# Performance work log

Measured on AMD Instinct MI355X. Metric: run time of the kernel, lower is better.

The kernel has to match this reference:

```python
import jax, jax.numpy as jnp
import numpy as np


def _consts():
    # Hypercube vertices: itertools.product([-1,1], repeat=n) order => MSB-first bits.
    def verts(nbits):
        idx = np.arange(2 ** nbits)
        return (((idx[:, None] >> np.arange(nbits - 1, -1, -1)[None, :]) & 1) * 2.0 - 1.0).astype(np.float32)

    hexagrams = verts(6)   # (64, 6)
    q2_verts = verts(2)    # (4, 2)
    q3_verts = verts(3)    # (8, 3)

    # Q2 vertex -> group one-hot, _Q2_TO_GROUP = [2, 1, 1, 0]
    q2_to_group = np.zeros((4, 3), dtype=np.float32)
    for v, g in enumerate([2, 1, 1, 0]):
        q2_to_group[v, g] = 1.0

    # Group anchors: ABSTRACT = mean(hex[63], hex[62]), DYNAMIC = mean(hex[19], hex[21]),
    # CONCRETE = mean(hex[0], hex[8]); then L2-normalized.
    anch = np.stack([
        hexagrams[[63, 62]].mean(0),
        hexagrams[[19, 21]].mean(0),
        hexagrams[[0, 8]].mean(0),
    ]).astype(np.float32)
    anch = anch / np.clip(np.linalg.norm(anch, axis=-1, keepdims=True), 1e-12, None)

    # Walsh-Hadamard popcount masks, pre-divided by their sums -> (64, 3) matrix.
    bits = np.array([bin(i).count('1') for i in range(64)], dtype=np.float32)
    wa = (bits >= 5).astype(np.float32)
    wd = (bits == 3).astype(np.float32)
    wc = (bits <= 1).astype(np.float32)
    wht_mat = np.stack([wa / wa.sum(), wd / wd.sum(), wc / wc.sum()], axis=1)

    return tuple(jnp.asarray(a) for a in (hexagrams, q2_verts, q3_verts, q2_to_group, anch, wht_mat))


def _q3_to_group_init():
    q3_map = np.zeros((8, 3), dtype=np.float32)
    for i in range(8):
        yc = bin(i).count('1')
        if yc == 0:
            q3_map[i, 2] = 1.0
        elif yc == 1:
            q3_map[i, 1] = 1.0
        elif yc == 2:
            q3_map[i, 0] = 0.6
            q3_map[i, 1] = 0.4
        else:
            q3_map[i, 0] = 1.0
    q3_map = q3_map / np.clip(q3_map.sum(axis=1, keepdims=True), 1e-8, None)
    return q3_map


def setup_inputs() -> dict:
    key = jax.random.key(0)
    k_x, k2, k3, k6 = jax.random.split(key, 4)
    B, T, D = 4, 4096, 2048
    s = 1.0 / float(np.sqrt(D))  # torch Linear default init range
    return {
        'x': jax.random.normal(k_x, (B, T, D), dtype=jnp.float32),
        'ln_w': jnp.ones((D,), dtype=jnp.float32),
        'ln_b': jnp.zeros((D,), dtype=jnp.float32),
        'w_q2': jax.random.uniform(k2, (2, D), minval=-s, maxval=s, dtype=jnp.float32),
        'w_q3': jax.random.uniform(k3, (3, D), minval=-s, maxval=s, dtype=jnp.float32),
        'w_q6': jax.random.uniform(k6, (6, D), minval=-s, maxval=s, dtype=jnp.float32),
        'log_temp': jnp.asarray(np.log(0.5), dtype=jnp.float32),
        'log_scale_mix': jnp.zeros((3,), dtype=jnp.float32),
        'q3_to_group': jnp.asarray(_q3_to_group_init()),
        'log_wht_mix': jnp.asarray(-2.0, dtype=jnp.float32),
    }


def _forward(x, ln_w, ln_b, w_q2, w_q3, w_q6, log_temp, log_scale_mix, q3_to_group, log_wht_mix):
    hexa, q2v, q3v, q2g, anch, wht_mat = _consts()

    # LayerNorm (eps = 1e-5, torch default)
    mu = x.mean(-1, keepdims=True)
    var = ((x - mu) ** 2).mean(-1, keepdims=True)
    h = (x - mu) * jax.lax.rsqrt(var + 1e-5) * ln_w + ln_b

    temp = jnp.clip(jnp.exp(log_temp), 0.1, 5.0)

    # Q2 scale: (B,T,2) -> 4 vertices -> 3 groups
    w2 = jax.nn.softmax(jnp.tanh(h @ w_q2.T) @ q2v.T / temp, axis=-1)
    score_q2 = w2 @ q2g

    # Q3 scale: (B,T,3) -> 8 vertices -> learned soft group map
    w3 = jax.nn.softmax(jnp.tanh(h @ w_q3.T) @ q3v.T / temp, axis=-1)
    score_q3 = w3 @ jax.nn.softmax(q3_to_group, axis=-1)

    # Q6 scale: (B,T,6) -> 64 hexagram vertices
    hex_w = jax.nn.softmax(jnp.tanh(h @ w_q6.T) @ hexa.T / temp, axis=-1)
    score_cos = (hex_w @ hexa) @ anch.T            # cosine-sim vs normalized anchors
    score_wht = hex_w @ wht_mat                    # popcount-mask averages
    alpha = jax.nn.sigmoid(log_wht_mix)
    score_q6 = (1.0 - alpha) * score_cos + alpha * score_wht

    mix = jax.nn.softmax(log_scale_mix)
    group_w = jax.nn.softmax(mix[0] * score_q2 + mix[1] * score_q3 + mix[2] * score_q6, axis=-1)

    mg = group_w.mean(axis=(0, 1))
    mh = hex_w.mean(axis=(0, 1))
    lb_loss = jnp.sum(mg * jnp.log(mg + 1e-8)) + 0.1 * jnp.sum(mh * jnp.log(mh + 1e-8))
    return group_w, hex_w, lb_loss


def reference(x, ln_w, ln_b, w_q2, w_q3, w_q6, log_temp, log_scale_mix, q3_to_group, log_wht_mix):
    return _forward(x, ln_w, ln_b, w_q2, w_q3, w_q6, log_temp, log_scale_mix, q3_to_group, log_wht_mix)
```

## Files before the change

### kernel.cpp

```cpp
#include <hip/hip_runtime.h>
#include <math.h>
#include <string.h>

#define D 2048
#define NTOK 16384
#define NROW 11
#define MROWS_U32 (NROW * D / 2)
#define K1_BLOCKS 2048
#define K1_THREADS 256
#define P1_ROWS 6
#define P2_ROWS 5
#define SW_U32 (P1_ROWS * 1024)

#define WS_A 0
#define WS_B 16
#define WS_IT 32
#define WS_ALPHA 33
#define WS_MIX 34
#define WS_M3 40
#define WS_MERGED 64
#define WS_PART (WS_MERGED + MROWS_U32)

typedef __fp16 h2 __attribute__((ext_vector_type(2)));

__device__ __forceinline__ float wsum(float v){
#pragma unroll
  for (int m = 1; m < 64; m <<= 1) v += __shfl_xor(v, m, 64);
  return v;
}
__device__ __forceinline__ float wmax(float v){
#pragma unroll
  for (int m = 1; m < 64; m <<= 1) v = fmaxf(v, __shfl_xor(v, m, 64));
  return v;
}
__device__ __forceinline__ float rcp_fast(float x){ return __builtin_amdgcn_rcpf(x); }
__device__ __forceinline__ float tanh_fast(float x){
  float e = __expf(2.0f * x);
  return 1.0f - 2.0f * rcp_fast(e + 1.0f);
}
__device__ __forceinline__ float sload(const float* __restrict__ p){
  return __uint_as_float(__builtin_amdgcn_readfirstlane(__float_as_uint(*p)));
}
__device__ __forceinline__ h2 u2h(unsigned int u){ h2 h; memcpy(&h, &u, 4); return h; }
__device__ __forceinline__ unsigned int h2u(h2 h){ unsigned int u; memcpy(&u, &h, 4); return u; }

__device__ __forceinline__ float fdot2(h2 a, h2 b, float c){
#if __has_builtin(__builtin_amdgcn_fdot2)
  return __builtin_amdgcn_fdot2(a, b, c, false);
#else
  return fmaf((float)a[0], (float)b[0], fmaf((float)a[1], (float)b[1], c));
#endif
}

__global__ __launch_bounds__(256) void k0_prep(
    const float* __restrict__ ln_w, const float* __restrict__ ln_b,
    const float* __restrict__ w_q2, const float* __restrict__ w_q3,
    const float* __restrict__ w_q6,
    const float* __restrict__ log_temp, const float* __restrict__ log_scale_mix,
    const float* __restrict__ q3_to_group, const float* __restrict__ log_wht_mix,
    float* __restrict__ ws)
{
  const int tid = threadIdx.x;
  const int k = blockIdx.x;
  unsigned int* wsu = (unsigned int*)ws;
  if (k < NROW){
    const float* row = (k < 2) ? (w_q2 + (size_t)k * D)
                     : (k < 5) ? (w_q3 + (size_t)(k - 2) * D)
                               : (w_q6 + (size_t)(k - 5) * D);
    float pa = 0.f, pb = 0.f;
    for (int i = tid * 2; i < D; i += 512){
      float w0 = row[i], w1 = row[i + 1];
      h2 h = __builtin_amdgcn_cvt_pkrtz(ln_w[i] * w0, ln_w[i + 1] * w1);
      pa += (float)h[0] + (float)h[1];
      pb = fmaf(ln_b[i], w0, pb);
      pb = fmaf(ln_b[i + 1], w1, pb);
      wsu[WS_MERGED + k * 1024 + i / 2] = h2u(h);
    }
    __shared__ float red[8];
    pa = wsum(pa); pb = wsum(pb);
    if ((tid & 63) == 0){ red[tid >> 6] = pa; red[4 + (tid >> 6)] = pb; }
    __syncthreads();
    if (tid == 0){
      ws[WS_A + k] = red[0] + red[1] + red[2] + red[3];
      ws[WS_B + k] = red[4] + red[5] + red[6] + red[7];
    }
  } else if (tid == 0){
    float t = __expf(log_temp[0]);
    t = fminf(fmaxf(t, 0.1f), 5.0f);
    ws[WS_IT] = 1.0f / t;
    ws[WS_ALPHA] = 1.0f / (1.0f + __expf(-log_wht_mix[0]));
    float m0 = log_scale_mix[0], m1 = log_scale_mix[1], m2 = log_scale_mix[2];
    float mm = fmaxf(m0, fmaxf(m1, m2));
    float e0 = __expf(m0 - mm), e1 = __expf(m1 - mm), e2 = __expf(m2 - mm);
    float inv = 1.0f / (e0 + e1 + e2);
    ws[WS_MIX + 0] = e0 * inv; ws[WS_MIX + 1] = e1 * inv; ws[WS_MIX + 2] = e2 * inv;
    for (int r = 0; r < 8; ++r){
      float v0 = q3_to_group[r*3+0], v1 = q3_to_group[r*3+1], v2 = q3_to_group[r*3+2];
      float mx = fmaxf(v0, fmaxf(v1, v2));
      float f0 = __expf(v0 - mx), f1 = __expf(v1 - mx), f2 = __expf(v2 - mx);
      float iv = 1.0f / (f0 + f1 + f2);
      ws[WS_M3 + r*3 + 0] = f0 * iv;
      ws[WS_M3 + r*3 + 1] = f1 * iv;
      ws[WS_M3 + r*3 + 2] = f2 * iv;
    }
  }
}

template<int NR>
__device__ __forceinline__ void dot_phase(const unsigned int* __restrict__ sW,
                                          const h2* __restrict__ xah,
                                          const h2* __restrict__ xbh,
                                          float* __restrict__ t0,
                                          float* __restrict__ t1, int lane){
#pragma unroll
  for (int c = 0; c < 8; ++c){
    const unsigned int* wb = sW + (c << 7) + lane * 2;
    const h2 a0 = xah[2*c], a1 = xah[2*c + 1];
    const h2 b0 = xbh[2*c], b1 = xbh[2*c + 1];
#pragma unroll
    for (int r = 0; r < NR; ++r){
      uint2 wu = *(const uint2*)(wb + (r << 10));
      h2 w0 = u2h(wu.x), w1 = u2h(wu.y);
      t0[r] = fdot2(a0, w0, t0[r]);
      t0[r] = fdot2(a1, w1, t0[r]);
      t1[r] = fdot2(b0, w0, t1[r]);
      t1[r] = fdot2(b1, w1, t1[r]);
    }
  }
}

__global__ __launch_bounds__(256) void k1_main(
    const float* __restrict__ x, const float* __restrict__ ws,
    float* __restrict__ gout, float* __restrict__ hout, float* __restrict__ part)
{
  __shared__ unsigned int sW[SW_U32];
  __shared__ float lred[4][68];
  const int tid  = threadIdx.x;
  const int lane = tid & 63;
  const int wid  = tid >> 6;
  const int blk  = blockIdx.x;
  const int tok0 = blk * 8 + wid * 2;

  const unsigned int* wsu = (const unsigned int*)ws + WS_MERGED;

  const float* xp0 = x + (size_t)tok0 * D + lane * 4;
  const float* xp1 = xp0 + D;
  float4 xa[8], xb[8];
#pragma unroll
  for (int i = 0; i < 8; ++i) xa[i] = *(const float4*)(xp0 + i * 256);
#pragma unroll
  for (int i = 0; i < 8; ++i) xb[i] = *(const float4*)(xp1 + i * 256);

  {
    const uint4* src = (const uint4*)wsu;
    uint4* dst = (uint4*)sW;
#pragma unroll
    for (int i = 0; i < 6; ++i) dst[tid + i * 256] = src[tid + i * 256];
  }

  float sum0 = 0.f, sum1 = 0.f, sq0 = 0.f, sq1 = 0.f;
  h2 xah[16], xbh[16];
#pragma unroll
  for (int i = 0; i < 8; ++i){
    float a0 = xa[i].x, a1 = xa[i].y, a2 = xa[i].z, a3 = xa[i].w;
    sum0 += (a0 + a1) + (a2 + a3);
    sq0 = fmaf(a0,a0, fmaf(a1,a1, fmaf(a2,a2, fmaf(a3,a3, sq0))));
    xah[2*i]   = __builtin_amdgcn_cvt_pkrtz(a0, a1);
    xah[2*i+1] = __builtin_amdgcn_cvt_pkrtz(a2, a3);
    float b0 = xb[i].x, b1 = xb[i].y, b2 = xb[i].z, b3 = xb[i].w;
    sum1 += (b0 + b1) + (b2 + b3);
    sq1 = fmaf(b0,b0, fmaf(b1,b1, fmaf(b2,b2, fmaf(b3,b3, sq1))));
    xbh[2*i]   = __builtin_amdgcn_cvt_pkrtz(b0, b1);
    xbh[2*i+1] = __builtin_amdgcn_cvt_pkrtz(b2, b3);
  }
  __syncthreads();

  float t0a[P1_ROWS], t1a[P1_ROWS];
#pragma unroll
  for (int r = 0; r < P1_ROWS; ++r){ t0a[r] = 0.f; t1a[r] = 0.f; }
  dot_phase<P1_ROWS>(sW, xah, xbh, t0a, t1a, lane);

  sum0 = wsum(sum0); sum1 = wsum(sum1);
  sq0  = wsum(sq0);  sq1  = wsum(sq1);
#pragma unroll
  for (int r = 0; r < P1_ROWS; ++r){ t0a[r] = wsum(t0a[r]); t1a[r] = wsum(t1a[r]); }

  __syncthreads();

  {
    const uint4* src = (const uint4*)(wsu + P1_ROWS * 1024);
    uint4* dst = (uint4*)sW;
#pragma unroll
    for (int i = 0; i < 5; ++i) dst[tid + i * 256] = src[tid + i * 256];
  }
  __syncthreads();

  float t0b[P2_ROWS], t1b[P2_ROWS];
#pragma unroll
  for (int r = 0; r < P2_ROWS; ++r){ t0b[r] = 0.f; t1b[r] = 0.f; }
  dot_phase<P2_ROWS>(sW, xah, xbh, t0b, t1b, lane);
#pragma unroll
  for (int r = 0; r < P2_ROWS; ++r){ t0b[r] = wsum(t0b[r]); t1b[r] = wsum(t1b[r]); }

  float a[NROW], bb[NROW];
#pragma unroll
  for (int k = 0; k < NROW; ++k){ a[k] = sload(ws + WS_A + k); bb[k] = sload(ws + WS_B + k); }
  const float it    = sload(ws + WS_IT);
  const float alpha = sload(ws + WS_ALPHA);
  const float mix0 = sload(ws + WS_MIX), mix1 = sload(ws + WS_MIX + 1), mix2 = sload(ws + WS_MIX + 2);
  float M3r[8][3];
#pragma unroll
  for (int r = 0; r < 8; ++r){
#pragma unroll
    for (int g = 0; g < 3; ++g) M3r[r][g] = sload(ws + WS_M3 + r*3 + g);
  }

  float sgn[6];
#pragma unroll
  for (int j = 0; j < 6; ++j) sgn[j] = ((lane >> (5 - j)) & 1) ? 1.0f : -1.0f;
  const float C5 = 0.44721359549995793f;
  const float A0c[6] = { C5,  C5,  C5,  C5,  C5, 0.f };
  const float A1c[6] = {-0.5f, 0.5f, -0.5f, 0.f, 0.f, 0.5f};
  const float A2c[6] = {-C5, -C5, 0.f, -C5, -C5, -C5};
  float cs0 = 0.f, cs1 = 0.f, cs2 = 0.f;
#pragma unroll
  for (int j = 0; j < 6; ++j){
    cs0 = fmaf(sgn[j], A0c[j], cs0);
    cs1 = fmaf(sgn[j], A1c[j], cs1);
    cs2 = fmaf(sgn[j], A2c[j], cs2);
  }
  const int pc = __popc(lane);
  const float w7c = 1.0f / 7.0f;
  float wh0 = (pc >= 5) ? w7c  : 0.f;
  float wh1 = (pc == 3) ? 0.05f: 0.f;
  float wh2 = (pc <= 1) ? w7c  : 0.f;
  const float m60 = (1.f - alpha)*cs0 + alpha*wh0;
  const float m61 = (1.f - alpha)*cs1 + alpha*wh1;
  const float m62 = (1.f - alpha)*cs2 + alpha*wh2;

  float hsum = 0.f, ga0 = 0.f, ga1 = 0.f, ga2 = 0.f;

#pragma unroll
  for (int j = 0; j < 2; ++j){
    const int tok = tok0 + j;
    const float sumj = j ? sum1 : sum0;
    const float sqj  = j ? sq1  : sq0;
    float mean = sumj * (1.0f / D);
    float var  = fmaf(sqj, 1.0f / D, -mean * mean);
    float rr   = rsqrtf(var + 1e-5f);
    float u[NROW];
#pragma unroll
    for (int k = 0; k < NROW; ++k){
      float tk = (k < P1_ROWS) ? (j ? t1a[k] : t0a[k]) : (j ? t1b[k - P1_ROWS] : t0b[k - P1_ROWS]);
      float d = fmaf(-mean, a[k], tk);
      u[k] = tanh_fast(fmaf(rr, d, bb[k]));
    }

    float p01 = u[0] + u[1], m01 = u[0] - u[1];
    float l0 = -p01*it, l1 = -m01*it, l2 = m01*it, l3 = p01*it;
    float mx2 = fmaxf(fmaxf(l0, l1), fmaxf(l2, l3));
    float e0 = __expf(l0-mx2), e1 = __expf(l1-mx2), e2 = __expf(l2-mx2), e3 = __expf(l3-mx2);
    float i2 = rcp_fast(e0 + e1 + e2 + e3);
    float s2g0 = e3 * i2, s2g1 = (e1 + e2) * i2, s2g2 = e0 * i2;

    float l3v[8]; float mx3 = -1e30f;
#pragma unroll
    for (int v = 0; v < 8; ++v){
      float acc = ((v & 4) ? u[2] : -u[2]) + ((v & 2) ? u[3] : -u[3]) + ((v & 1) ? u[4] : -u[4]);
      l3v[v] = acc * it;
      mx3 = fmaxf(mx3, l3v[v]);
    }
    float w3v[8]; float se3 = 0.f;
#pragma unroll
    for (int v = 0; v < 8; ++v){ w3v[v] = __expf(l3v[v] - mx3); se3 += w3v[v]; }
    float i3 = rcp_fast(se3);
    float s3g0 = 0.f, s3g1 = 0.f, s3g2 = 0.f;
#pragma unroll
    for (int v = 0; v < 8; ++v){
      s3g0 = fmaf(w3v[v], M3r[v][0], s3g0);
      s3g1 = fmaf(w3v[v], M3r[v][1], s3g1);
      s3g2 = fmaf(w3v[v], M3r[v][2], s3g2);
    }
    s3g0 *= i3; s3g1 *= i3; s3g2 *= i3;

    float lg = 0.f;
#pragma unroll
    for (int jj = 0; jj < 6; ++jj) lg = fmaf(sgn[jj], u[5 + jj], lg);
    lg *= it;
    float mx6 = wmax(lg);
    float p   = __expf(lg - mx6);
    float se6 = wsum(p);
    float hw  = p * rcp_fast(se6);
    hout[(size_t)tok * 64 + lane] = hw;
    hsum += hw;
    float s6g0 = wsum(hw * m60);
    float s6g1 = wsum(hw * m61);
    float s6g2 = wsum(hw * m62);

    float g0 = mix0*s2g0 + mix1*s3g0 + mix2*s6g0;
    float g1 = mix0*s2g1 + mix1*s3g1 + mix2*s6g1;
    float g2 = mix0*s2g2 + mix1*s3g2 + mix2*s6g2;
    float gm = fmaxf(g0, fmaxf(g1, g2));
    float y0 = __expf(g0-gm), y1 = __expf(g1-gm), y2 = __expf(g2-gm);
    float gi = rcp_fast(y0 + y1 + y2);
    float gw0 = y0*gi, gw1 = y1*gi, gw2 = y2*gi;
    ga0 += gw0; ga1 += gw1; ga2 += gw2;
    if (lane < 3){
      float val = (lane == 0) ? gw0 : (lane == 1) ? gw1 : gw2;
      gout[(size_t)tok * 3 + lane] = val;
    }
  }

  lred[wid][lane] = hsum;
  if (lane < 3){
    float val = (lane == 0) ? ga0 : (lane == 1) ? ga1 : ga2;
    lred[wid][64 + lane] = val;
  }
  __syncthreads();
  if (tid < 67){
    float v = lred[0][tid] + lred[1][tid] + lred[2][tid] + lred[3][tid];
    part[(size_t)tid * K1_BLOCKS + blk] = v;
  }
}

__global__ __launch_bounds__(1024) void k2_loss(const float* __restrict__ part,
                                                float* __restrict__ lout)
{
  __shared__ float sums[68];
  const int tid = threadIdx.x;
  const int lane = tid & 63;
  const int wid  = tid >> 6;
  for (int jv = wid; jv < 67; jv += 16){
    const float4* p = (const float4*)(part + (size_t)jv * K1_BLOCKS);
    float v = 0.f;
#pragma unroll
    for (int b = 0; b < K1_BLOCKS / 256; ++b){
      float4 q = p[lane + b * 64];
      v += (q.x + q.y) + (q.z + q.w);
    }
    v = wsum(v);
    if (lane == 0) sums[jv] = v;
  }
  __syncthreads();
  if (wid == 0){
    const float inv = 1.0f / (float)NTOK;
    float mh = sums[lane] * inv;
    float term = 0.1f * mh * logf(mh + 1e-8f);
    if (lane < 3){
      float mg = sums[64 + lane] * inv;
      term += mg * logf(mg + 1e-8f);
    }
    float L = wsum(term);
    if (lane == 0) lout[0] = L;
  }
}

extern "C" void kernel_launch(void* const* d_in, const int* in_sizes, int n_in,
                              void* d_out, int out_size, void* d_ws, size_t ws_size,
                              hipStream_t stream)
{
  const float* x             = (const float*)d_in[0];
  const float* ln_w          = (const float*)d_in[1];
  const float* ln_b          = (const float*)d_in[2];
  const float* w_q2          = (const float*)d_in[3];
  const float* w_q3          = (const float*)d_in[4];
  const float* w_q6          = (const float*)d_in[5];
  const float* log_temp      = (const float*)d_in[6];
  const float* log_scale_mix = (const float*)d_in[7];
  const float* q3_to_group   = (const float*)d_in[8];
  const float* log_wht_mix   = (const float*)d_in[9];

  float* out  = (float*)d_out;
  float* gout = out;
  float* hout = out + (size_t)NTOK * 3;
  float* lout = out + (size_t)NTOK * 3 + (size_t)NTOK * 64;
  float* ws   = (float*)d_ws;

  k0_prep<<<12, 256, 0, stream>>>(ln_w, ln_b, w_q2, w_q3, w_q6,
                                  log_temp, log_scale_mix, q3_to_group, log_wht_mix, ws);
  k1_main<<<K1_BLOCKS, K1_THREADS, 0, stream>>>(x, ws, gout, hout, ws + WS_PART);
  k2_loss<<<1, 1024, 0, stream>>>(ws + WS_PART, lout);
}
```

Measured before the change: 53.75 us.

## Stage all weight rows once per block and process four tokens per wave

New measurement: 69.28 us. 1.29x slower.

```diff
diff --git a/kernel.cpp b/kernel.cpp
--- a/kernel.cpp
+++ b/kernel.cpp
@@ -6,11 +6,8 @@
 #define NTOK 16384
 #define NROW 11
 #define MROWS_U32 (NROW * D / 2)
-#define K1_BLOCKS 2048
+#define K1_BLOCKS 1024
 #define K1_THREADS 256
-#define P1_ROWS 6
-#define P2_ROWS 5
-#define SW_U32 (P1_ROWS * 1024)
 
 #define WS_A 0
 #define WS_B 16
@@ -106,25 +103,42 @@
   }
 }
 
-template<int NR>
-__device__ __forceinline__ void dot_phase(const unsigned int* __restrict__ sW,
-                                          const h2* __restrict__ xah,
-                                          const h2* __restrict__ xbh,
-                                          float* __restrict__ t0,
-                                          float* __restrict__ t1, int lane){
-#pragma unroll
-  for (int c = 0; c < 8; ++c){
-    const unsigned int* wb = sW + (c << 7) + lane * 2;
-    const h2 a0 = xah[2*c], a1 = xah[2*c + 1];
-    const h2 b0 = xbh[2*c], b1 = xbh[2*c + 1];
-#pragma unroll
-    for (int r = 0; r < NR; ++r){
-      uint2 wu = *(const uint2*)(wb + (r << 10));
-      h2 w0 = u2h(wu.x), w1 = u2h(wu.y);
-      t0[r] = fdot2(a0, w0, t0[r]);
-      t0[r] = fdot2(a1, w1, t0[r]);
-      t1[r] = fdot2(b0, w0, t1[r]);
-      t1[r] = fdot2(b1, w1, t1[r]);
+__device__ __forceinline__ void load_row(const float* __restrict__ p, float4* f){
+#pragma unroll
+  for (int c = 0; c < 4; ++c){
+    f[2*c]     = *(const float4*)(p + c * 512);
+    f[2*c + 1] = *(const float4*)(p + c * 512 + 4);
+  }
+}
+__device__ __forceinline__ void cvt_row(const float4* __restrict__ f, h2* __restrict__ h,
+                                        float& sum, float& sq){
+#pragma unroll
+  for (int i = 0; i < 8; ++i){
+    float a0 = f[i].x, a1 = f[i].y, a2 = f[i].z, a3 = f[i].w;
+    sum += (a0 + a1) + (a2 + a3);
+    sq = fmaf(a0,a0, fmaf(a1,a1, fmaf(a2,a2, fmaf(a3,a3, sq))));
+    h[2*i]   = __builtin_amdgcn_cvt_pkrtz(a0, a1);
+    h[2*i+1] = __builtin_amdgcn_cvt_pkrtz(a2, a3);
+  }
+}
+
+template<int R0, int R1>
+__device__ __forceinline__ void dot_rows(const unsigned int* __restrict__ sW,
+                                         const h2* __restrict__ hx,
+                                         const h2* __restrict__ hy,
+                                         float* __restrict__ t0,
+                                         float* __restrict__ t1, int lane){
+#pragma unroll
+  for (int c = 0; c < 4; ++c){
+    const unsigned int* wb = sW + (c << 8) + lane * 4;
+    const h2 x0 = hx[4*c], x1 = hx[4*c+1], x2 = hx[4*c+2], x3 = hx[4*c+3];
+    const h2 y0 = hy[4*c], y1 = hy[4*c+1], y2 = hy[4*c+2], y3 = hy[4*c+3];
+#pragma unroll
+    for (int k = R0; k < R1; ++k){
+      uint4 wq = *(const uint4*)(wb + (k << 10));
+      h2 w0 = u2h(wq.x), w1 = u2h(wq.y), w2 = u2h(wq.z), w3 = u2h(wq.w);
+      t0[k] = fdot2(x3, w3, fdot2(x2, w2, fdot2(x1, w1, fdot2(x0, w0, t0[k]))));
+      t1[k] = fdot2(y3, w3, fdot2(y2, w2, fdot2(y1, w1, fdot2(y0, w0, t1[k]))));
     }
   }
 }
@@ -133,74 +147,57 @@
     const float* __restrict__ x, const float* __restrict__ ws,
     float* __restrict__ gout, float* __restrict__ hout, float* __restrict__ part)
 {
-  __shared__ unsigned int sW[SW_U32];
+  __shared__ unsigned int sW[MROWS_U32];
   __shared__ float lred[4][68];
   const int tid  = threadIdx.x;
   const int lane = tid & 63;
   const int wid  = tid >> 6;
   const int blk  = blockIdx.x;
-  const int tok0 = blk * 8 + wid * 2;
-
-  const unsigned int* wsu = (const unsigned int*)ws + WS_MERGED;
-
-  const float* xp0 = x + (size_t)tok0 * D + lane * 4;
-  const float* xp1 = xp0 + D;
-  float4 xa[8], xb[8];
-#pragma unroll
-  for (int i = 0; i < 8; ++i) xa[i] = *(const float4*)(xp0 + i * 256);
-#pragma unroll
-  for (int i = 0; i < 8; ++i) xb[i] = *(const float4*)(xp1 + i * 256);
+  const int tok0 = blk * 16 + wid * 4;
+
+  const float* xp = x + (size_t)tok0 * D + lane * 8;
+
+  float4 fA0[8], fA1[8];
+  load_row(xp, fA0);
+  load_row(xp + D, fA1);
 
   {
-    const uint4* src = (const uint4*)wsu;
+    const uint4* src = (const uint4*)((const unsigned int*)ws + WS_MERGED);
     uint4* dst = (uint4*)sW;
 #pragma unroll
-    for (int i = 0; i < 6; ++i) dst[tid + i * 256] = src[tid + i * 256];
-  }
-
-  float sum0 = 0.f, sum1 = 0.f, sq0 = 0.f, sq1 = 0.f;
-  h2 xah[16], xbh[16];
-#pragma unroll
-  for (int i = 0; i < 8; ++i){
-    float a0 = xa[i].x, a1 = xa[i].y, a2 = xa[i].z, a3 = xa[i].w;
-    sum0 += (a0 + a1) + (a2 + a3);
-    sq0 = fmaf(a0,a0, fmaf(a1,a1, fmaf(a2,a2, fmaf(a3,a3, sq0))));
-    xah[2*i]   = __builtin_amdgcn_cvt_pkrtz(a0, a1);
-    xah[2*i+1] = __builtin_amdgcn_cvt_pkrtz(a2, a3);
-    float b0 = xb[i].x, b1 = xb[i].y, b2 = xb[i].z, b3 = xb[i].w;
-    sum1 += (b0 + b1) + (b2 + b3);
-    sq1 = fmaf(b0,b0, fmaf(b1,b1, fmaf(b2,b2, fmaf(b3,b3, sq1))));
-    xbh[2*i]   = __builtin_amdgcn_cvt_pkrtz(b0, b1);
-    xbh[2*i+1] = __builtin_amdgcn_cvt_pkrtz(b2, b3);
+    for (int i = 0; i < 11; ++i) dst[tid + i * 256] = src[tid + i * 256];
   }
   __syncthreads();
 
-  float t0a[P1_ROWS], t1a[P1_ROWS];
-#pragma unroll
-  for (int r = 0; r < P1_ROWS; ++r){ t0a[r] = 0.f; t1a[r] = 0.f; }
-  dot_phase<P1_ROWS>(sW, xah, xbh, t0a, t1a, lane);
-
-  sum0 = wsum(sum0); sum1 = wsum(sum1);
-  sq0  = wsum(sq0);  sq1  = wsum(sq1);
-#pragma unroll
-  for (int r = 0; r < P1_ROWS; ++r){ t0a[r] = wsum(t0a[r]); t1a[r] = wsum(t1a[r]); }
-
-  __syncthreads();
-
-  {
-    const uint4* src = (const uint4*)(wsu + P1_ROWS * 1024);
-    uint4* dst = (uint4*)sW;
-#pragma unroll
-    for (int i = 0; i < 5; ++i) dst[tid + i * 256] = src[tid + i * 256];
-  }
-  __syncthreads();
-
-  float t0b[P2_ROWS], t1b[P2_ROWS];
-#pragma unroll
-  for (int r = 0; r < P2_ROWS; ++r){ t0b[r] = 0.f; t1b[r] = 0.f; }
-  dot_phase<P2_ROWS>(sW, xah, xbh, t0b, t1b, lane);
-#pragma unroll
-  for (int r = 0; r < P2_ROWS; ++r){ t0b[r] = wsum(t0b[r]); t1b[r] = wsum(t1b[r]); }
+  float sA0 = 0.f, qA0 = 0.f, sA1 = 0.f, qA1 = 0.f;
+  h2 hA0[16], hA1[16];
+  cvt_row(fA0, hA0, sA0, qA0);
+  cvt_row(fA1, hA1, sA1, qA1);
+
+  float4 fB0[8];
+  load_row(xp + 2 * D, fB0);
+
+  float tA0[NROW], tA1[NROW];
+#pragma unroll
+  for (int k = 0; k < NROW; ++k){ tA0[k] = 0.f; tA1[k] = 0.f; }
+
+  dot_rows<0, 6>(sW, hA0, hA1, tA0, tA1, lane);
+
+  float sB0 = 0.f, qB0 = 0.f;
+  h2 hB0[16];
+  cvt_row(fB0, hB0, sB0, qB0);
+  float4 fB1[8];
+  load_row(xp + 3 * D, fB1);
+
+  dot_rows<6, NROW>(sW, hA0, hA1, tA0, tA1, lane);
+
+  sA0 = wsum(sA0); qA0 = wsum(qA0); sA1 = wsum(sA1); qA1 = wsum(qA1);
+#pragma unroll
+  for (int k = 0; k < NROW; ++k){ tA0[k] = wsum(tA0[k]); tA1[k] = wsum(tA1[k]); }
+
+  float sB1 = 0.f, qB1 = 0.f;
+  h2 hB1[16];
+  cvt_row(fB1, hB1, sB1, qB1);
 
   float a[NROW], bb[NROW];
 #pragma unroll
@@ -240,76 +237,85 @@
 
   float hsum = 0.f, ga0 = 0.f, ga1 = 0.f, ga2 = 0.f;
 
-#pragma unroll
-  for (int j = 0; j < 2; ++j){
-    const int tok = tok0 + j;
-    const float sumj = j ? sum1 : sum0;
-    const float sqj  = j ? sq1  : sq0;
-    float mean = sumj * (1.0f / D);
-    float var  = fmaf(sqj, 1.0f / D, -mean * mean);
-    float rr   = rsqrtf(var + 1e-5f);
-    float u[NROW];
-#pragma unroll
-    for (int k = 0; k < NROW; ++k){
-      float tk = (k < P1_ROWS) ? (j ? t1a[k] : t0a[k]) : (j ? t1b[k - P1_ROWS] : t0b[k - P1_ROWS]);
-      float d = fmaf(-mean, a[k], tk);
-      u[k] = tanh_fast(fmaf(rr, d, bb[k]));
-    }
-
-    float p01 = u[0] + u[1], m01 = u[0] - u[1];
-    float l0 = -p01*it, l1 = -m01*it, l2 = m01*it, l3 = p01*it;
-    float mx2 = fmaxf(fmaxf(l0, l1), fmaxf(l2, l3));
-    float e0 = __expf(l0-mx2), e1 = __expf(l1-mx2), e2 = __expf(l2-mx2), e3 = __expf(l3-mx2);
-    float i2 = rcp_fast(e0 + e1 + e2 + e3);
-    float s2g0 = e3 * i2, s2g1 = (e1 + e2) * i2, s2g2 = e0 * i2;
-
-    float l3v[8]; float mx3 = -1e30f;
-#pragma unroll
-    for (int v = 0; v < 8; ++v){
-      float acc = ((v & 4) ? u[2] : -u[2]) + ((v & 2) ? u[3] : -u[3]) + ((v & 1) ? u[4] : -u[4]);
-      l3v[v] = acc * it;
-      mx3 = fmaxf(mx3, l3v[v]);
-    }
-    float w3v[8]; float se3 = 0.f;
-#pragma unroll
-    for (int v = 0; v < 8; ++v){ w3v[v] = __expf(l3v[v] - mx3); se3 += w3v[v]; }
-    float i3 = rcp_fast(se3);
-    float s3g0 = 0.f, s3g1 = 0.f, s3g2 = 0.f;
-#pragma unroll
-    for (int v = 0; v < 8; ++v){
-      s3g0 = fmaf(w3v[v], M3r[v][0], s3g0);
-      s3g1 = fmaf(w3v[v], M3r[v][1], s3g1);
-      s3g2 = fmaf(w3v[v], M3r[v][2], s3g2);
-    }
-    s3g0 *= i3; s3g1 *= i3; s3g2 *= i3;
-
-    float lg = 0.f;
-#pragma unroll
-    for (int jj = 0; jj < 6; ++jj) lg = fmaf(sgn[jj], u[5 + jj], lg);
-    lg *= it;
-    float mx6 = wmax(lg);
-    float p   = __expf(lg - mx6);
-    float se6 = wsum(p);
-    float hw  = p * rcp_fast(se6);
-    hout[(size_t)tok * 64 + lane] = hw;
-    hsum += hw;
-    float s6g0 = wsum(hw * m60);
-    float s6g1 = wsum(hw * m61);
-    float s6g2 = wsum(hw * m62);
-
-    float g0 = mix0*s2g0 + mix1*s3g0 + mix2*s6g0;
-    float g1 = mix0*s2g1 + mix1*s3g1 + mix2*s6g1;
-    float g2 = mix0*s2g2 + mix1*s3g2 + mix2*s6g2;
-    float gm = fmaxf(g0, fmaxf(g1, g2));
-    float y0 = __expf(g0-gm), y1 = __expf(g1-gm), y2 = __expf(g2-gm);
-    float gi = rcp_fast(y0 + y1 + y2);
-    float gw0 = y0*gi, gw1 = y1*gi, gw2 = y2*gi;
-    ga0 += gw0; ga1 += gw1; ga2 += gw2;
-    if (lane < 3){
-      float val = (lane == 0) ? gw0 : (lane == 1) ? gw1 : gw2;
-      gout[(size_t)tok * 3 + lane] = val;
-    }
-  }
+#define TOKEN_EPILOGUE(TOK, SUMJ, SQJ, TARR)                                         \
+  {                                                                                  \
+    const int tok = (TOK);                                                           \
+    float mean = (SUMJ) * (1.0f / D);                                                \
+    float var  = fmaf((SQJ), 1.0f / D, -mean * mean);                                \
+    float rr   = rsqrtf(var + 1e-5f);                                                \
+    float u[NROW];                                                                   \
+    _Pragma("unroll")                                                                \
+    for (int k = 0; k < NROW; ++k){                                                  \
+      float d = fmaf(-mean, a[k], (TARR)[k]);                                        \
+      u[k] = tanh_fast(fmaf(rr, d, bb[k]));                                          \
+    }                                                                                \
+    float p01 = u[0] + u[1], m01 = u[0] - u[1];                                      \
+    float l0 = -p01*it, l1 = -m01*it, l2 = m01*it, l3 = p01*it;                      \
+    float mx2 = fmaxf(fmaxf(l0, l1), fmaxf(l2, l3));                                 \
+    float e0 = __expf(l0-mx2), e1 = __expf(l1-mx2), e2 = __expf(l2-mx2), e3 = __expf(l3-mx2); \
+    float i2 = rcp_fast(e0 + e1 + e2 + e3);                                          \
+    float s2g0 = e3 * i2, s2g1 = (e1 + e2) * i2, s2g2 = e0 * i2;                     \
+    float l3v[8]; float mx3 = -1e30f;                                                \
+    _Pragma("unroll")                                                                \
+    for (int v = 0; v < 8; ++v){                                                     \
+      float acc = ((v & 4) ? u[2] : -u[2]) + ((v & 2) ? u[3] : -u[3]) + ((v & 1) ? u[4] : -u[4]); \
+      l3v[v] = acc * it;                                                             \
+      mx3 = fmaxf(mx3, l3v[v]);                                                      \
+    }                                                                                \
+    float w3v[8]; float se3 = 0.f;                                                   \
+    _Pragma("unroll")                                                                \
+    for (int v = 0; v < 8; ++v){ w3v[v] = __expf(l3v[v] - mx3); se3 += w3v[v]; }     \
+    float i3 = rcp_fast(se3);                                                        \
+    float s3g0 = 0.f, s3g1 = 0.f, s3g2 = 0.f;                                        \
+    _Pragma("unroll")                                                                \
+    for (int v = 0; v < 8; ++v){                                                     \
+      s3g0 = fmaf(w3v[v], M3r[v][0], s3g0);                                          \
+      s3g1 = fmaf(w3v[v], M3r[v][1], s3g1);                                          \
+      s3g2 = fmaf(w3v[v], M3r[v][2], s3g2);                                          \
+    }                                                                                \
+    s3g0 *= i3; s3g1 *= i3; s3g2 *= i3;                                              \
+    float lg = 0.f;                                                                  \
+    _Pragma("unroll")                                                                \
+    for (int jj = 0; jj < 6; ++jj) lg = fmaf(sgn[jj], u[5 + jj], lg);                \
+    lg *= it;                                                                        \
+    float mx6 = wmax(lg);                                                            \
+    float p   = __expf(lg - mx6);                                                    \
+    float se6 = wsum(p);                                                             \
+    float hw  = p * rcp_fast(se6);                                                   \
+    hout[(size_t)tok * 64 + lane] = hw;                                              \
+    hsum += hw;                                                                      \
+    float s6g0 = wsum(hw * m60);                                                     \
+    float s6g1 = wsum(hw * m61);                                                     \
+    float s6g2 = wsum(hw * m62);                                                     \
+    float g0 = mix0*s2g0 + mix1*s3g0 + mix2*s6g0;                                    \
+    float g1 = mix0*s2g1 + mix1*s3g1 + mix2*s6g1;                                    \
+    float g2 = mix0*s2g2 + mix1*s3g2 + mix2*s6g2;                                    \
+    float gm = fmaxf(g0, fmaxf(g1, g2));                                             \
+    float y0 = __expf(g0-gm), y1 = __expf(g1-gm), y2 = __expf(g2-gm);                \
+    float gi = rcp_fast(y0 + y1 + y2);                                               \
+    float gw0 = y0*gi, gw1 = y1*gi, gw2 = y2*gi;                                     \
+    ga0 += gw0; ga1 += gw1; ga2 += gw2;                                              \
+    if (lane < 3){                                                                   \
+      float val = (lane == 0) ? gw0 : (lane == 1) ? gw1 : gw2;                       \
+      gout[(size_t)tok * 3 + lane] = val;                                            \
+    }                                                                                \
+  }
+
+  TOKEN_EPILOGUE(tok0 + 0, sA0, qA0, tA0)
+  TOKEN_EPILOGUE(tok0 + 1, sA1, qA1, tA1)
+
+  float tB0[NROW], tB1[NROW];
+#pragma unroll
+  for (int k = 0; k < NROW; ++k){ tB0[k] = 0.f; tB1[k] = 0.f; }
+  dot_rows<0, NROW>(sW, hB0, hB1, tB0, tB1, lane);
+
+  sB0 = wsum(sB0); qB0 = wsum(qB0); sB1 = wsum(sB1); qB1 = wsum(qB1);
+#pragma unroll
+  for (int k = 0; k < NROW; ++k){ tB0[k] = wsum(tB0[k]); tB1[k] = wsum(tB1[k]); }
+
+  TOKEN_EPILOGUE(tok0 + 2, sB0, qB0, tB0)
+  TOKEN_EPILOGUE(tok0 + 3, sB1, qB1, tB1)
+#undef TOKEN_EPILOGUE
 
   lred[wid][lane] = hsum;
   if (lane < 3){
```

## Use atomic partial accumulation and wider per-lane x loads with 128-bit weight reads

Applied to the files above, without the earlier changes.

Result: slower. 76.71 us (+42.7%).

```diff
diff --git a/kernel.cpp b/kernel.cpp
--- a/kernel.cpp
+++ b/kernel.cpp
@@ -19,7 +19,7 @@
 #define WS_MIX 34
 #define WS_M3 40
 #define WS_MERGED 64
-#define WS_PART (WS_MERGED + MROWS_U32)
+#define WS_ACC (WS_MERGED + MROWS_U32)
 
 typedef __fp16 h2 __attribute__((ext_vector_type(2)));
 
@@ -84,54 +84,74 @@
       ws[WS_A + k] = red[0] + red[1] + red[2] + red[3];
       ws[WS_B + k] = red[4] + red[5] + red[6] + red[7];
     }
-  } else if (tid == 0){
-    float t = __expf(log_temp[0]);
-    t = fminf(fmaxf(t, 0.1f), 5.0f);
-    ws[WS_IT] = 1.0f / t;
-    ws[WS_ALPHA] = 1.0f / (1.0f + __expf(-log_wht_mix[0]));
-    float m0 = log_scale_mix[0], m1 = log_scale_mix[1], m2 = log_scale_mix[2];
-    float mm = fmaxf(m0, fmaxf(m1, m2));
-    float e0 = __expf(m0 - mm), e1 = __expf(m1 - mm), e2 = __expf(m2 - mm);
-    float inv = 1.0f / (e0 + e1 + e2);
-    ws[WS_MIX + 0] = e0 * inv; ws[WS_MIX + 1] = e1 * inv; ws[WS_MIX + 2] = e2 * inv;
-    for (int r = 0; r < 8; ++r){
-      float v0 = q3_to_group[r*3+0], v1 = q3_to_group[r*3+1], v2 = q3_to_group[r*3+2];
-      float mx = fmaxf(v0, fmaxf(v1, v2));
-      float f0 = __expf(v0 - mx), f1 = __expf(v1 - mx), f2 = __expf(v2 - mx);
-      float iv = 1.0f / (f0 + f1 + f2);
-      ws[WS_M3 + r*3 + 0] = f0 * iv;
-      ws[WS_M3 + r*3 + 1] = f1 * iv;
-      ws[WS_M3 + r*3 + 2] = f2 * iv;
-    }
+  } else {
+    if (tid < 67) ws[WS_ACC + tid] = 0.f;
+    if (tid == 0){
+      float t = __expf(log_temp[0]);
+      t = fminf(fmaxf(t, 0.1f), 5.0f);
+      ws[WS_IT] = 1.0f / t;
+      ws[WS_ALPHA] = 1.0f / (1.0f + __expf(-log_wht_mix[0]));
+      float m0 = log_scale_mix[0], m1 = log_scale_mix[1], m2 = log_scale_mix[2];
+      float mm = fmaxf(m0, fmaxf(m1, m2));
+      float e0 = __expf(m0 - mm), e1 = __expf(m1 - mm), e2 = __expf(m2 - mm);
+      float inv = 1.0f / (e0 + e1 + e2);
+      ws[WS_MIX + 0] = e0 * inv; ws[WS_MIX + 1] = e1 * inv; ws[WS_MIX + 2] = e2 * inv;
+      for (int r = 0; r < 8; ++r){
+        float v0 = q3_to_group[r*3+0], v1 = q3_to_group[r*3+1], v2 = q3_to_group[r*3+2];
+        float mx = fmaxf(v0, fmaxf(v1, v2));
+        float f0 = __expf(v0 - mx), f1 = __expf(v1 - mx), f2 = __expf(v2 - mx);
+        float iv = 1.0f / (f0 + f1 + f2);
+        ws[WS_M3 + r*3 + 0] = f0 * iv;
+        ws[WS_M3 + r*3 + 1] = f1 * iv;
+        ws[WS_M3 + r*3 + 2] = f2 * iv;
+      }
+    }
+  }
+}
+
+__device__ __forceinline__ void load_row(const float* __restrict__ p, float4* f){
+#pragma unroll
+  for (int c = 0; c < 4; ++c){
+    f[2*c]     = *(const float4*)(p + c * 512);
+    f[2*c + 1] = *(const float4*)(p + c * 512 + 4);
+  }
+}
+__device__ __forceinline__ void cvt_row(const float4* __restrict__ f, h2* __restrict__ h,
+                                        float& sum, float& sq){
+#pragma unroll
+  for (int i = 0; i < 8; ++i){
+    float a0 = f[i].x, a1 = f[i].y, a2 = f[i].z, a3 = f[i].w;
+    sum += (a0 + a1) + (a2 + a3);
+    sq = fmaf(a0,a0, fmaf(a1,a1, fmaf(a2,a2, fmaf(a3,a3, sq))));
+    h[2*i]   = __builtin_amdgcn_cvt_pkrtz(a0, a1);
+    h[2*i+1] = __builtin_amdgcn_cvt_pkrtz(a2, a3);
   }
 }
 
 template<int NR>
 __device__ __forceinline__ void dot_phase(const unsigned int* __restrict__ sW,
-                                          const h2* __restrict__ xah,
-                                          const h2* __restrict__ xbh,
+                                          const h2* __restrict__ hx,
+                                          const h2* __restrict__ hy,
                                           float* __restrict__ t0,
                                           float* __restrict__ t1, int lane){
 #pragma unroll
-  for (int c = 0; c < 8; ++c){
-    const unsigned int* wb = sW + (c << 7) + lane * 2;
-    const h2 a0 = xah[2*c], a1 = xah[2*c + 1];
-    const h2 b0 = xbh[2*c], b1 = xbh[2*c + 1];
+  for (int c = 0; c < 4; ++c){
+    const unsigned int* wb = sW + (c << 8) + lane * 4;
+    const h2 x0 = hx[4*c], x1 = hx[4*c+1], x2 = hx[4*c+2], x3 = hx[4*c+3];
+    const h2 y0 = hy[4*c], y1 = hy[4*c+1], y2 = hy[4*c+2], y3 = hy[4*c+3];
 #pragma unroll
     for (int r = 0; r < NR; ++r){
-      uint2 wu = *(const uint2*)(wb + (r << 10));
-      h2 w0 = u2h(wu.x), w1 = u2h(wu.y);
-      t0[r] = fdot2(a0, w0, t0[r]);
-      t0[r] = fdot2(a1, w1, t0[r]);
-      t1[r] = fdot2(b0, w0, t1[r]);
-      t1[r] = fdot2(b1, w1, t1[r]);
+      uint4 wq = *(const uint4*)(wb + (r << 10));
+      h2 w0 = u2h(wq.x), w1 = u2h(wq.y), w2 = u2h(wq.z), w3 = u2h(wq.w);
+      t0[r] = fdot2(x3, w3, fdot2(x2, w2, fdot2(x1, w1, fdot2(x0, w0, t0[r]))));
+      t1[r] = fdot2(y3, w3, fdot2(y2, w2, fdot2(y1, w1, fdot2(y0, w0, t1[r]))));
     }
   }
 }
 
 __global__ __launch_bounds__(256) void k1_main(
     const float* __restrict__ x, const float* __restrict__ ws,
-    float* __restrict__ gout, float* __restrict__ hout, float* __restrict__ part)
+    float* __restrict__ gout, float* __restrict__ hout, float* __restrict__ acc)
 {
   __shared__ unsigned int sW[SW_U32];
   __shared__ float lred[4][68];
@@ -143,13 +163,11 @@
 
   const unsigned int* wsu = (const unsigned int*)ws + WS_MERGED;
 
-  const float* xp0 = x + (size_t)tok0 * D + lane * 4;
+  const float* xp0 = x + (size_t)tok0 * D + lane * 8;
   const float* xp1 = xp0 + D;
   float4 xa[8], xb[8];
-#pragma unroll
-  for (int i = 0; i < 8; ++i) xa[i] = *(const float4*)(xp0 + i * 256);
-#pragma unroll
-  for (int i = 0; i < 8; ++i) xb[i] = *(const float4*)(xp1 + i * 256);
+  load_row(xp0, xa);
+  load_row(xp1, xb);
 
   {
     const uint4* src = (const uint4*)wsu;
@@ -160,19 +178,8 @@
 
   float sum0 = 0.f, sum1 = 0.f, sq0 = 0.f, sq1 = 0.f;
   h2 xah[16], xbh[16];
-#pragma unroll
-  for (int i = 0; i < 8; ++i){
-    float a0 = xa[i].x, a1 = xa[i].y, a2 = xa[i].z, a3 = xa[i].w;
-    sum0 += (a0 + a1) + (a2 + a3);
-    sq0 = fmaf(a0,a0, fmaf(a1,a1, fmaf(a2,a2, fmaf(a3,a3, sq0))));
-    xah[2*i]   = __builtin_amdgcn_cvt_pkrtz(a0, a1);
-    xah[2*i+1] = __builtin_amdgcn_cvt_pkrtz(a2, a3);
-    float b0 = xb[i].x, b1 = xb[i].y, b2 = xb[i].z, b3 = xb[i].w;
-    sum1 += (b0 + b1) + (b2 + b3);
-    sq1 = fmaf(b0,b0, fmaf(b1,b1, fmaf(b2,b2, fmaf(b3,b3, sq1))));
-    xbh[2*i]   = __builtin_amdgcn_cvt_pkrtz(b0, b1);
-    xbh[2*i+1] = __builtin_amdgcn_cvt_pkrtz(b2, b3);
-  }
+  cvt_row(xa, xah, sum0, sq0);
+  cvt_row(xb, xbh, sum1, sq1);
   __syncthreads();
 
   float t0a[P1_ROWS], t1a[P1_ROWS];
@@ -266,8 +273,8 @@
     float l3v[8]; float mx3 = -1e30f;
 #pragma unroll
     for (int v = 0; v < 8; ++v){
-      float acc = ((v & 4) ? u[2] : -u[2]) + ((v & 2) ? u[3] : -u[3]) + ((v & 1) ? u[4] : -u[4]);
-      l3v[v] = acc * it;
+      float acc3 = ((v & 4) ? u[2] : -u[2]) + ((v & 2) ? u[3] : -u[3]) + ((v & 1) ? u[4] : -u[4]);
+      l3v[v] = acc3 * it;
       mx3 = fmaxf(mx3, l3v[v]);
     }
     float w3v[8]; float se3 = 0.f;
@@ -319,40 +326,23 @@
   __syncthreads();
   if (tid < 67){
     float v = lred[0][tid] + lred[1][tid] + lred[2][tid] + lred[3][tid];
-    part[(size_t)tid * K1_BLOCKS + blk] = v;
-  }
-}
-
-__global__ __launch_bounds__(1024) void k2_loss(const float* __restrict__ part,
-                                                float* __restrict__ lout)
+    atomicAdd(&acc[tid], v);
+  }
+}
+
+__global__ __launch_bounds__(64) void k2_loss(const float* __restrict__ acc,
+                                              float* __restrict__ lout)
 {
-  __shared__ float sums[68];
-  const int tid = threadIdx.x;
-  const int lane = tid & 63;
-  const int wid  = tid >> 6;
-  for (int jv = wid; jv < 67; jv += 16){
-    const float4* p = (const float4*)(part + (size_t)jv * K1_BLOCKS);
-    float v = 0.f;
-#pragma unroll
-    for (int b = 0; b < K1_BLOCKS / 256; ++b){
-      float4 q = p[lane + b * 64];
-      v += (q.x + q.y) + (q.z + q.w);
-    }
-    v = wsum(v);
-    if (lane == 0) sums[jv] = v;
-  }
-  __syncthreads();
-  if (wid == 0){
-    const float inv = 1.0f / (float)NTOK;
-    float mh = sums[lane] * inv;
-    float term = 0.1f * mh * logf(mh + 1e-8f);
-    if (lane < 3){
-      float mg = sums[64 + lane] * inv;
-      term += mg * logf(mg + 1e-8f);
-    }
-    float L = wsum(term);
-    if (lane == 0) lout[0] = L;
-  }
+  const int lane = threadIdx.x;
+  const float inv = 1.0f / (float)NTOK;
+  float mh = acc[lane] * inv;
+  float term = 0.1f * mh * logf(mh + 1e-8f);
+  if (lane < 3){
+    float mg = acc[64 + lane] * inv;
+    term += mg * logf(mg + 1e-8f);
+  }
+  float L = wsum(term);
+  if (lane == 0) lout[0] = L;
 }
 
 extern "C" void kernel_launch(void* const* d_in, const int* in_sizes, int n_in,
@@ -378,6 +368,6 @@
 
   k0_prep<<<12, 256, 0, stream>>>(ln_w, ln_b, w_q2, w_q3, w_q6,
                                   log_temp, log_scale_mix, q3_to_group, log_wht_mix, ws);
-  k1_main<<<K1_BLOCKS, K1_THREADS, 0, stream>>>(x, ws, gout, hout, ws + WS_PART);
-  k2_loss<<<1, 1024, 0, stream>>>(ws + WS_PART, lout);
-}
+  k1_main<<<K1_BLOCKS, K1_THREADS, 0, stream>>>(x, ws, gout, hout, ws + WS_ACC);
+  k2_loss<<<1, 64, 0, stream>>>(ws + WS_ACC, lout);
+}
```

## Stage all weight rows in LDS once with larger 512-thread blocks

Applied to the files above, without the earlier changes.

New measurement: 53.87 us. No clear change (+0.2%).

```diff
diff --git a/kernel.cpp b/kernel.cpp
--- a/kernel.cpp
+++ b/kernel.cpp
@@ -6,11 +6,8 @@
 #define NTOK 16384
 #define NROW 11
 #define MROWS_U32 (NROW * D / 2)
-#define K1_BLOCKS 2048
-#define K1_THREADS 256
-#define P1_ROWS 6
-#define P2_ROWS 5
-#define SW_U32 (P1_ROWS * 1024)
+#define K1_BLOCKS 1024
+#define K1_THREADS 512
 
 #define WS_A 0
 #define WS_B 16
@@ -106,40 +103,17 @@
   }
 }
 
-template<int NR>
-__device__ __forceinline__ void dot_phase(const unsigned int* __restrict__ sW,
-                                          const h2* __restrict__ xah,
-                                          const h2* __restrict__ xbh,
-                                          float* __restrict__ t0,
-                                          float* __restrict__ t1, int lane){
-#pragma unroll
-  for (int c = 0; c < 8; ++c){
-    const unsigned int* wb = sW + (c << 7) + lane * 2;
-    const h2 a0 = xah[2*c], a1 = xah[2*c + 1];
-    const h2 b0 = xbh[2*c], b1 = xbh[2*c + 1];
-#pragma unroll
-    for (int r = 0; r < NR; ++r){
-      uint2 wu = *(const uint2*)(wb + (r << 10));
-      h2 w0 = u2h(wu.x), w1 = u2h(wu.y);
-      t0[r] = fdot2(a0, w0, t0[r]);
-      t0[r] = fdot2(a1, w1, t0[r]);
-      t1[r] = fdot2(b0, w0, t1[r]);
-      t1[r] = fdot2(b1, w1, t1[r]);
-    }
-  }
-}
-
-__global__ __launch_bounds__(256) void k1_main(
+__global__ __launch_bounds__(512) void k1_main(
     const float* __restrict__ x, const float* __restrict__ ws,
     float* __restrict__ gout, float* __restrict__ hout, float* __restrict__ part)
 {
-  __shared__ unsigned int sW[SW_U32];
-  __shared__ float lred[4][68];
+  __shared__ unsigned int sW[MROWS_U32];
+  __shared__ float lred[8][68];
   const int tid  = threadIdx.x;
   const int lane = tid & 63;
   const int wid  = tid >> 6;
   const int blk  = blockIdx.x;
-  const int tok0 = blk * 8 + wid * 2;
+  const int tok0 = blk * 16 + wid * 2;
 
   const unsigned int* wsu = (const unsigned int*)ws + WS_MERGED;
 
@@ -155,7 +129,10 @@
     const uint4* src = (const uint4*)wsu;
     uint4* dst = (uint4*)sW;
 #pragma unroll
-    for (int i = 0; i < 6; ++i) dst[tid + i * 256] = src[tid + i * 256];
+    for (int i = 0; i < 6; ++i){
+      int idx = tid + i * 512;
+      if (idx < MROWS_U32 / 4) dst[idx] = src[idx];
+    }
   }
 
   float sum0 = 0.f, sum1 = 0.f, sq0 = 0.f, sq1 = 0.f;
@@ -175,32 +152,27 @@
   }
   __syncthreads();
 
-  float t0a[P1_ROWS], t1a[P1_ROWS];
-#pragma unroll
-  for (int r = 0; r < P1_ROWS; ++r){ t0a[r] = 0.f; t1a[r] = 0.f; }
-  dot_phase<P1_ROWS>(sW, xah, xbh, t0a, t1a, lane);
+  float t0[NROW], t1[NROW];
+#pragma unroll
+  for (int r = 0; r < NROW; ++r){ t0[r] = 0.f; t1[r] = 0.f; }
+#pragma unroll
+  for (int c = 0; c < 8; ++c){
+    const unsigned int* wb = sW + (c << 7) + lane * 2;
+    const h2 a0 = xah[2*c], a1 = xah[2*c + 1];
+    const h2 b0 = xbh[2*c], b1 = xbh[2*c + 1];
+#pragma unroll
+    for (int k = 0; k < NROW; ++k){
+      uint2 wu = *(const uint2*)(wb + (k << 10));
+      h2 w0 = u2h(wu.x), w1 = u2h(wu.y);
+      t0[k] = fdot2(a1, w1, fdot2(a0, w0, t0[k]));
+      t1[k] = fdot2(b1, w1, fdot2(b0, w0, t1[k]));
+    }
+  }
 
   sum0 = wsum(sum0); sum1 = wsum(sum1);
   sq0  = wsum(sq0);  sq1  = wsum(sq1);
 #pragma unroll
-  for (int r = 0; r < P1_ROWS; ++r){ t0a[r] = wsum(t0a[r]); t1a[r] = wsum(t1a[r]); }
-
-  __syncthreads();
-
-  {
-    const uint4* src = (const uint4*)(wsu + P1_ROWS * 1024);
-    uint4* dst = (uint4*)sW;
-#pragma unroll
-    for (int i = 0; i < 5; ++i) dst[tid + i * 256] = src[tid + i * 256];
-  }
-  __syncthreads();
-
-  float t0b[P2_ROWS], t1b[P2_ROWS];
-#pragma unroll
-  for (int r = 0; r < P2_ROWS; ++r){ t0b[r] = 0.f; t1b[r] = 0.f; }
-  dot_phase<P2_ROWS>(sW, xah, xbh, t0b, t1b, lane);
-#pragma unroll
-  for (int r = 0; r < P2_ROWS; ++r){ t0b[r] = wsum(t0b[r]); t1b[r] = wsum(t1b[r]); }
+  for (int k = 0; k < NROW; ++k){ t0[k] = wsum(t0[k]); t1[k] = wsum(t1[k]); }
 
   float a[NROW], bb[NROW];
 #pragma unroll
@@ -251,7 +223,7 @@
     float u[NROW];
 #pragma unroll
     for (int k = 0; k < NROW; ++k){
-      float tk = (k < P1_ROWS) ? (j ? t1a[k] : t0a[k]) : (j ? t1b[k - P1_ROWS] : t0b[k - P1_ROWS]);
+      float tk = j ? t1[k] : t0[k];
       float d = fmaf(-mean, a[k], tk);
       u[k] = tanh_fast(fmaf(rr, d, bb[k]));
     }
@@ -266,8 +238,8 @@
     float l3v[8]; float mx3 = -1e30f;
 #pragma unroll
     for (int v = 0; v < 8; ++v){
-      float acc = ((v & 4) ? u[2] : -u[2]) + ((v & 2) ? u[3] : -u[3]) + ((v & 1) ? u[4] : -u[4]);
-      l3v[v] = acc * it;
+      float acc3 = ((v & 4) ? u[2] : -u[2]) + ((v & 2) ? u[3] : -u[3]) + ((v & 1) ? u[4] : -u[4]);
+      l3v[v] = acc3 * it;
       mx3 = fmaxf(mx3, l3v[v]);
     }
     float w3v[8]; float se3 = 0.f;
@@ -318,7 +290,9 @@
   }
   __syncthreads();
   if (tid < 67){
-    float v = lred[0][tid] + lred[1][tid] + lred[2][tid] + lred[3][tid];
+    float v = 0.f;
+#pragma unroll
+    for (int r = 0; r < 8; ++r) v += lred[r][tid];
     part[(size_t)tid * K1_BLOCKS + blk] = v;
   }
 }
```
